# Kernel tuning notes

Hardware: AMD Instinct MI355X
Metric: run time of the kernel (lower is better)

The kernel has to match this reference:

```python
import jax, jax.numpy as jnp
import numpy as np

N, DEG = 20000, 16          # nodes, fixed neighbor-list length
H, C, D, IN = 4, 16, 128, 256  # cluster_heads, num_centroids, hidden_dim, input_dim
NEG_SLOPE = 0.2


def setup_inputs() -> dict:
    key = jax.random.key(0)
    ks = jax.random.split(key, 12)
    s_in = 1.0 / np.sqrt(IN)
    s_h = 1.0 / np.sqrt(D)
    inp = {
        "x_node": jax.random.normal(ks[0], (N, IN), dtype=jnp.float32),
        "adj": jax.random.randint(ks[1], (N, DEG), 0, N, dtype=jnp.int32),
        "epoch": 1,
        # linear layers (torch convention: W [out, in])
        "W1": jax.random.uniform(ks[2], (D, IN), jnp.float32, -s_in, s_in),
        "b1": jax.random.uniform(ks[3], (D,), jnp.float32, -s_in, s_in),
        "W2": jax.random.uniform(ks[4], (D, D), jnp.float32, -s_h, s_h),
        "b2": jax.random.uniform(ks[5], (D,), jnp.float32, -s_h, s_h),
        "W21": jax.random.uniform(ks[6], (D, D), jnp.float32, -s_h, s_h),
        "b21": jax.random.uniform(ks[7], (D,), jnp.float32, -s_h, s_h),
        # centroids: 2*rand-1, shape [H, C*D]
        "centroids": 2.0 * jax.random.uniform(ks[8], (H, C * D), dtype=jnp.float32) - 1.0,
        # headConv: xavier_uniform gain=1.414 on [H, 1]
        "headConv": jax.random.uniform(ks[9], (H, 1), jnp.float32,
                                       -1.414 * np.sqrt(6.0 / (H + 1)),
                                       1.414 * np.sqrt(6.0 / (H + 1))),
    }
    return inp


def _leaky(x):
    return jnp.where(x >= 0, x, NEG_SLOPE * x)


def _cluster_block(h, adj, centroids, headConv):
    # h: [N, D]; adj: [N, deg]; centroids: [H, C*D]; headConv: [H, 1]
    cent = centroids.reshape(H, C, D)
    # squared L2 distance dist[h,c,n] = ||x_n - cent_hc||^2 (norm expansion,
    # avoids the [H,C,N,D] broadcast the torch code materializes)
    hn2 = jnp.sum(h * h, axis=-1)                      # [N]
    cn2 = jnp.sum(cent * cent, axis=-1)                # [H, C]
    cross = jnp.einsum('hcd,nd->hcn', cent, h)         # [H, C, N]
    dist = cn2[..., None] + hn2[None, None, :] - 2.0 * cross
    # nu=1: q = (1 + dist)^-1
    q = 1.0 / (1.0 + dist)                             # [H, C, N]
    # gather neighbor scores per node and normalize over the edge dim
    qn = q[:, :, adj]                                  # [H, C, N, deg]
    qn = qn / jnp.sum(qn, axis=3, keepdims=True)
    # combine heads with headConv, then softmax over edges per centroid
    w = jnp.einsum('hcne,h->nce', qn, headConv[:, 0])  # [N, C, deg]
    w = jax.nn.softmax(w, axis=2)
    # weighted aggregation of neighbor features
    new_feat = jnp.einsum('nce,ned->ncd', w, h[adj])   # [N, C, D]
    return new_feat


def reference(x_node, adj, epoch, W1, b1, W2, b2, W21, b21, centroids, headConv):
    # eval mode: dropout is identity
    x = _leaky(x_node @ W1.T + b1)
    h_prime = _leaky(x @ W2.T + b2)                    # [N, D]
    new_feat = _cluster_block(h_prime, adj, centroids, headConv)
    new_feat = _leaky(new_feat @ W21.T + b21)          # [N, C, D]
    return (h_prime, new_feat)
```

## Files before the change

kernel.cpp:

```cpp
#include <hip/hip_runtime.h>
#include <cstdint>
#include <cstddef>

#define NEG_SLOPE 0.2f

typedef __attribute__((ext_vector_type(8))) short bf16x8;
typedef __attribute__((ext_vector_type(8))) unsigned short u16x8;
typedef __attribute__((ext_vector_type(4))) unsigned short u16x4;
typedef __attribute__((ext_vector_type(4))) float f32x4;
typedef __attribute__((ext_vector_type(2))) float f32x2;

__device__ __forceinline__ float leaky_f(float x) { return x >= 0.f ? x : NEG_SLOPE * x; }

__device__ __forceinline__ unsigned short f2bf(float f) {
    union { float f; uint32_t u; } v; v.f = f;
    return (unsigned short)((v.u + 0x7fffu + ((v.u >> 16) & 1u)) >> 16);
}
__device__ __forceinline__ float bf2f(unsigned short u) {
    union { uint32_t u; float f; } v; v.u = ((uint32_t)u) << 16; return v.f;
}
__device__ __forceinline__ float bfhi(uint32_t w) {
    union { uint32_t u; float f; } v; v.u = w & 0xffff0000u; return v.f;
}
__device__ __forceinline__ float bflo(uint32_t w) {
    union { uint32_t u; float f; } v; v.u = w << 16; return v.f;
}
__device__ __forceinline__ u16x8 cvt8(float4 a, float4 b) {
    u16x8 o;
    o[0] = f2bf(a.x); o[1] = f2bf(a.y); o[2] = f2bf(a.z); o[3] = f2bf(a.w);
    o[4] = f2bf(b.x); o[5] = f2bf(b.y); o[6] = f2bf(b.z); o[7] = f2bf(b.w);
    return o;
}

#if __has_builtin(__builtin_elementwise_fma)
__device__ __forceinline__ f32x2 fma2(f32x2 a, f32x2 b, f32x2 c) {
    return __builtin_elementwise_fma(a, b, c);
}
#else
__device__ __forceinline__ f32x2 fma2(f32x2 a, f32x2 b, f32x2 c) {
    f32x2 r; r[0] = fmaf(a[0], b[0], c[0]); r[1] = fmaf(a[1], b[1], c[1]); return r;
}
#endif

__device__ __forceinline__ float xor32_add(float v) {
    float y = v;
    asm volatile("v_permlane32_swap_b32 %0, %1" : "+v"(y), "+v"(v));
    return v + y;
}

__global__ __launch_bounds__(256)
void pack_kernel(const float* __restrict__ x_node, const float* __restrict__ W1,
                 const float* __restrict__ W2, const float* __restrict__ W21,
                 const float* __restrict__ cent,
                 unsigned short* __restrict__ xb, unsigned short* __restrict__ pw1,
                 unsigned short* __restrict__ pw2, unsigned short* __restrict__ pw3,
                 float* __restrict__ cn2g, int N)
{
    const int bid = blockIdx.x, tid = threadIdx.x;
    if (bid < 36) {
        const int sub = tid >> 6, lane = tid & 63, g = bid * 4 + sub;
        const int l15 = lane & 15, l4 = lane >> 4;
        const float* src; unsigned short* dst;
        if (g < 64) {
            int step = g >> 3, f = g & 7;
            src = W1 + (size_t)(f * 16 + l15) * 256 + step * 32 + l4 * 8;
            dst = pw1 + ((size_t)(step * 8 + f) * 64 + lane) * 8;
        } else if (g < 96) {
            int gg = g - 64, step = gg >> 3, f = gg & 7;
            src = W2 + (size_t)(f * 16 + l15) * 128 + step * 32 + l4 * 8;
            dst = pw2 + ((size_t)(step * 8 + f) * 64 + lane) * 8;
        } else {
            int gg = g - 96, step = gg / 12, f = gg % 12;
            int brow = f * 16 + l15;
            const float* base = (brow < 128) ? (W21 + (size_t)brow * 128)
                                             : (cent + (size_t)(brow - 128) * 128);
            src = base + step * 32 + l4 * 8;
            dst = pw3 + ((size_t)(step * 12 + f) * 64 + lane) * 8;
        }
        float4 a = *reinterpret_cast<const float4*>(src);
        float4 b = *reinterpret_cast<const float4*>(src + 4);
        *reinterpret_cast<u16x8*>(dst) = cvt8(a, b);
    } else if (bid == 36) {
        int r = tid >> 2, c0 = (tid & 3) * 32;
        const float* cr = cent + (size_t)r * 128 + c0;
        float s = 0.f;
#pragma unroll
        for (int q = 0; q < 8; q++) {
            float4 v = *reinterpret_cast<const float4*>(cr + q * 4);
            s += v.x * v.x + v.y * v.y + v.z * v.z + v.w * v.w;
        }
        s += __shfl_xor(s, 1); s += __shfl_xor(s, 2);
        if ((tid & 3) == 0) cn2g[r] = s;
    } else {
        size_t base = (size_t)(bid - 37) * 4096 + (size_t)tid * 16;
        float4 v0 = *reinterpret_cast<const float4*>(x_node + base);
        float4 v1 = *reinterpret_cast<const float4*>(x_node + base + 4);
        float4 v2 = *reinterpret_cast<const float4*>(x_node + base + 8);
        float4 v3 = *reinterpret_cast<const float4*>(x_node + base + 12);
        *reinterpret_cast<u16x8*>(xb + base)     = cvt8(v0, v1);
        *reinterpret_cast<u16x8*>(xb + base + 8) = cvt8(v2, v3);
    }
}

__global__ __launch_bounds__(256)
void fused_gemms(const unsigned short* __restrict__ xb,
                 const unsigned short* __restrict__ pw1, const unsigned short* __restrict__ pw2,
                 const unsigned short* __restrict__ pw3,
                 const float* __restrict__ b1, const float* __restrict__ b2,
                 const float* __restrict__ cn2g,
                 float* __restrict__ h_out, unsigned short* __restrict__ hWb,
                 unsigned short* __restrict__ qtb, int N)
{
    __shared__ __align__(16) short Xs[16 * 136];
    __shared__ __align__(16) float hf32[16 * 132];
    __shared__ __align__(16) unsigned short hWs[16 * 136];
    __shared__ __align__(16) unsigned short qts[16 * 72];
    __shared__ float hn2s[4][16];

    const int tid = threadIdx.x, wave = tid >> 6, lane = tid & 63;
    const int l15 = lane & 15, l4 = lane >> 4;
    const int rowBlk = blockIdx.x * 16;

    f32x4 a0{0.f,0.f,0.f,0.f}, a1{0.f,0.f,0.f,0.f}, a2{0.f,0.f,0.f,0.f};
    {
        const unsigned short* ap = xb + (size_t)(rowBlk + l15) * 256 + l4 * 8;
        const unsigned short* bp = pw1 + (size_t)(wave * 2) * 512 + lane * 8;
#pragma unroll
        for (int k = 0; k < 8; k++) {
            bf16x8 af = *reinterpret_cast<const bf16x8*>(ap + k * 32);
            bf16x8 bf0 = *reinterpret_cast<const bf16x8*>(bp + (size_t)k * 8 * 512);
            bf16x8 bf1 = *reinterpret_cast<const bf16x8*>(bp + (size_t)k * 8 * 512 + 512);
            a0 = __builtin_amdgcn_mfma_f32_16x16x32_bf16(af, bf0, a0, 0, 0, 0);
            a1 = __builtin_amdgcn_mfma_f32_16x16x32_bf16(af, bf1, a1, 0, 0, 0);
        }
        float bia = b1[wave * 32 + l15], bib = b1[wave * 32 + 16 + l15];
#pragma unroll
        for (int j = 0; j < 4; j++) {
            Xs[(l4 * 4 + j) * 136 + wave * 32 + l15]      = (short)f2bf(leaky_f(a0[j] + bia));
            Xs[(l4 * 4 + j) * 136 + wave * 32 + 16 + l15] = (short)f2bf(leaky_f(a1[j] + bib));
        }
    }
    __syncthreads();

    a0 = f32x4{0.f,0.f,0.f,0.f}; a1 = f32x4{0.f,0.f,0.f,0.f};
    const short* xp = &Xs[l15 * 136 + l4 * 8];
    {
        const unsigned short* bp = pw2 + (size_t)(wave * 2) * 512 + lane * 8;
#pragma unroll
        for (int k = 0; k < 4; k++) {
            bf16x8 af = *reinterpret_cast<const bf16x8*>(xp + k * 32);
            bf16x8 bf0 = *reinterpret_cast<const bf16x8*>(bp + (size_t)k * 8 * 512);
            bf16x8 bf1 = *reinterpret_cast<const bf16x8*>(bp + (size_t)k * 8 * 512 + 512);
            a0 = __builtin_amdgcn_mfma_f32_16x16x32_bf16(af, bf0, a0, 0, 0, 0);
            a1 = __builtin_amdgcn_mfma_f32_16x16x32_bf16(af, bf1, a1, 0, 0, 0);
        }
    }
    float hv0[4], hv1[4], pn[4];
    {
        float bia = b2[wave * 32 + l15], bib = b2[wave * 32 + 16 + l15];
#pragma unroll
        for (int j = 0; j < 4; j++) {
            hv0[j] = leaky_f(a0[j] + bia);
            hv1[j] = leaky_f(a1[j] + bib);
            float s = hv0[j] * hv0[j] + hv1[j] * hv1[j];
            s += __shfl_xor(s, 1); s += __shfl_xor(s, 2);
            s += __shfl_xor(s, 4); s += __shfl_xor(s, 8);
            pn[j] = s;
        }
    }
    __syncthreads();

#pragma unroll
    for (int j = 0; j < 4; j++) {
        int r = l4 * 4 + j;
        hf32[r * 132 + wave * 32 + l15]      = hv0[j];
        hf32[r * 132 + wave * 32 + 16 + l15] = hv1[j];
        Xs[r * 136 + wave * 32 + l15]      = (short)f2bf(hv0[j]);
        Xs[r * 136 + wave * 32 + 16 + l15] = (short)f2bf(hv1[j]);
        if (l15 == 0) hn2s[wave][r] = pn[j];
    }
    __syncthreads();

    {
        int r = tid >> 4, c0 = (tid & 15) * 8;
        f32x4 v0 = *reinterpret_cast<const f32x4*>(&hf32[r * 132 + c0]);
        f32x4 v1 = *reinterpret_cast<const f32x4*>(&hf32[r * 132 + c0 + 4]);
        float* dst = h_out + (size_t)(rowBlk + r) * 128 + c0;
        __builtin_nontemporal_store(v0, reinterpret_cast<f32x4*>(dst));
        __builtin_nontemporal_store(v1, reinterpret_cast<f32x4*>(dst + 4));
    }

    a0 = f32x4{0.f,0.f,0.f,0.f}; a1 = f32x4{0.f,0.f,0.f,0.f}; a2 = f32x4{0.f,0.f,0.f,0.f};
    {
        const unsigned short* bp = pw3 + (size_t)(wave * 3) * 512 + lane * 8;
#pragma unroll
        for (int k = 0; k < 4; k++) {
            bf16x8 af = *reinterpret_cast<const bf16x8*>(xp + k * 32);
            bf16x8 bf0 = *reinterpret_cast<const bf16x8*>(bp + (size_t)k * 12 * 512);
            bf16x8 bf1 = *reinterpret_cast<const bf16x8*>(bp + (size_t)k * 12 * 512 + 512);
            bf16x8 bf2 = *reinterpret_cast<const bf16x8*>(bp + (size_t)k * 12 * 512 + 1024);
            a0 = __builtin_amdgcn_mfma_f32_16x16x32_bf16(af, bf0, a0, 0, 0, 0);
            a1 = __builtin_amdgcn_mfma_f32_16x16x32_bf16(af, bf1, a1, 0, 0, 0);
            a2 = __builtin_amdgcn_mfma_f32_16x16x32_bf16(af, bf2, a2, 0, 0, 0);
        }
    }
    {
        float hn2r[4];
#pragma unroll
        for (int j = 0; j < 4; j++)
            hn2r[j] = hn2s[0][l4 * 4 + j] + hn2s[1][l4 * 4 + j]
                    + hn2s[2][l4 * 4 + j] + hn2s[3][l4 * 4 + j];
        f32x4 av[3] = {a0, a1, a2};
#pragma unroll
        for (int ff = 0; ff < 3; ff++) {
            int col = wave * 48 + ff * 16 + l15;
            if (col < 128) {
#pragma unroll
                for (int j = 0; j < 4; j++)
                    hWs[(l4 * 4 + j) * 136 + col] = f2bf(av[ff][j]);
            } else {
                int c2 = col - 128;
                float cn2v = cn2g[c2];
#pragma unroll
                for (int j = 0; j < 4; j++) {
                    float q = 1.f / (1.f + cn2v + hn2r[j] - 2.f * av[ff][j]);
                    qts[(l4 * 4 + j) * 72 + c2] = f2bf(q);
                }
            }
        }
    }
    __syncthreads();

    {
        int r = tid >> 4, c0 = (tid & 15) * 8;
        *reinterpret_cast<u16x8*>(hWb + (size_t)(rowBlk + r) * 128 + c0) =
            *reinterpret_cast<const u16x8*>(&hWs[r * 136 + c0]);
        int cq = (tid & 15) * 4;
        *reinterpret_cast<u16x4*>(qtb + (size_t)(rowBlk + r) * 64 + cq) =
            *reinterpret_cast<const u16x4*>(&qts[r * 72 + cq]);
    }
}

struct PerWaveU {
    union {
        unsigned short qs[1024];
        float wbuf[16][16];
    };
};

__global__ __launch_bounds__(256)
void agg_kernel(const int* __restrict__ adj, const unsigned short* __restrict__ qtb,
                const unsigned short* __restrict__ hWb, const float* __restrict__ b21,
                const float* __restrict__ headConv, float* __restrict__ out1)
{
    __shared__ __align__(16) unsigned short hs[4][16 * 128];
    __shared__ __align__(16) PerWaveU upw[4];

    const int wv = threadIdx.x >> 6, lane = threadIdx.x & 63;
    const int eg = lane >> 4, l15 = lane & 15;
    const int n = blockIdx.x * 4 + wv;

    const int myadj = adj[n * 16 + l15];

#pragma unroll
    for (int i = 0; i < 2; i++) {
        int row = i * 8 + (lane >> 3);
        int nb = __shfl(myadj, row);
        *reinterpret_cast<u16x8*>(&upw[wv].qs[i * 512 + lane * 8]) =
            *reinterpret_cast<const u16x8*>(qtb + (size_t)nb * 64 + (lane & 7) * 8);
    }
#pragma unroll
    for (int i = 0; i < 4; i++) {
        int row = i * 4 + eg;
        int nb = __shfl(myadj, row);
        *reinterpret_cast<u16x8*>(&hs[wv][i * 512 + lane * 8]) =
            *reinterpret_cast<const u16x8*>(hWb + (size_t)nb * 128 + l15 * 8);
    }

    {
        float qv[16];
        float s = 0.f;
#pragma unroll
        for (int e = 0; e < 16; e++) { qv[e] = bf2f(upw[wv].qs[e * 64 + lane]); s += qv[e]; }
        float rs = 1.f / s;
        float conv = headConv[eg];
        float ex[4] = {0.f, 0.f, 0.f, 0.f};
#pragma unroll
        for (int e = 0; e < 16; e++) {
            float v = conv * qv[e] * rs;
            v += __shfl_xor(v, 16);
            v = xor32_add(v);
            float evv = __expf(v);
            bool mine = (eg == (e >> 2));
            ex[e & 3] = mine ? evv : ex[e & 3];
        }
        float ps = ex[0] + ex[1] + ex[2] + ex[3];
        ps += __shfl_xor(ps, 16);
        ps = xor32_add(ps);
        float inv = 1.f / ps;
#pragma unroll
        for (int j = 0; j < 4; j++) upw[wv].wbuf[eg * 4 + j][l15] = ex[j] * inv;
    }

    {
        const int d0 = l15 * 4;
        float bvf[8];
        *reinterpret_cast<float4*>(bvf)     = *reinterpret_cast<const float4*>(b21 + d0);
        *reinterpret_cast<float4*>(bvf + 4) = *reinterpret_cast<const float4*>(b21 + d0 + 64);
        f32x2 acc2[4][4];
#pragma unroll
        for (int jc = 0; jc < 4; jc++) {
            acc2[jc][0] = f32x2{bvf[0], bvf[1]};
            acc2[jc][1] = f32x2{bvf[2], bvf[3]};
            acc2[jc][2] = f32x2{bvf[4], bvf[5]};
            acc2[jc][3] = f32x2{bvf[6], bvf[7]};
        }

#pragma unroll
        for (int e = 0; e < 16; e++) {
            uint2 wlo = *reinterpret_cast<const uint2*>(&hs[wv][e * 128 + d0]);
            uint2 whi = *reinterpret_cast<const uint2*>(&hs[wv][e * 128 + 64 + d0]);
            float w4[4];
            *reinterpret_cast<float4*>(w4) =
                *reinterpret_cast<const float4*>(&upw[wv].wbuf[e][eg * 4]);
            f32x2 hv2[4];
            hv2[0] = f32x2{bflo(wlo.x), bfhi(wlo.x)};
            hv2[1] = f32x2{bflo(wlo.y), bfhi(wlo.y)};
            hv2[2] = f32x2{bflo(whi.x), bfhi(whi.x)};
            hv2[3] = f32x2{bflo(whi.y), bfhi(whi.y)};
#pragma unroll
            for (int jc = 0; jc < 4; jc++) {
                f32x2 w2 = f32x2{w4[jc], w4[jc]};
#pragma unroll
                for (int q = 0; q < 4; q++)
                    acc2[jc][q] = fma2(w2, hv2[q], acc2[jc][q]);
            }
        }

#pragma unroll
        for (int jc = 0; jc < 4; jc++) {
            f32x4 lo, hi;
            lo[0] = leaky_f(acc2[jc][0][0]); lo[1] = leaky_f(acc2[jc][0][1]);
            lo[2] = leaky_f(acc2[jc][1][0]); lo[3] = leaky_f(acc2[jc][1][1]);
            hi[0] = leaky_f(acc2[jc][2][0]); hi[1] = leaky_f(acc2[jc][2][1]);
            hi[2] = leaky_f(acc2[jc][3][0]); hi[3] = leaky_f(acc2[jc][3][1]);
            float* dst = out1 + ((size_t)(n * 16 + eg * 4 + jc)) * 128;
            __builtin_nontemporal_store(lo, reinterpret_cast<f32x4*>(dst + d0));
            __builtin_nontemporal_store(hi, reinterpret_cast<f32x4*>(dst + d0 + 64));
        }
    }
}

extern "C" void kernel_launch(void* const* d_in, const int* in_sizes, int n_in,
                              void* d_out, int out_size, void* d_ws, size_t ws_size,
                              hipStream_t stream)
{
    const float* x_node   = (const float*)d_in[0];
    const int*   adj      = (const int*)  d_in[1];
    const float* W1       = (const float*)d_in[3];
    const float* b1       = (const float*)d_in[4];
    const float* W2       = (const float*)d_in[5];
    const float* b2       = (const float*)d_in[6];
    const float* W21      = (const float*)d_in[7];
    const float* b21      = (const float*)d_in[8];
    const float* cent     = (const float*)d_in[9];
    const float* headConv = (const float*)d_in[10];

    const int N = in_sizes[0] / 256;

    float* h    = (float*)d_out;
    float* out1 = h + (size_t)N * 128;

    unsigned short* xb  = (unsigned short*)d_ws;
    unsigned short* hWb = xb  + (size_t)N * 256;
    unsigned short* qtb = hWb + (size_t)N * 128;
    unsigned short* pw1 = qtb + (size_t)N * 64;
    unsigned short* pw2 = pw1 + 32768;
    unsigned short* pw3 = pw2 + 16384;
    float*          cn2g = (float*)(pw3 + 24576);

    const int xblocks = (N * 256) / 4096;

    pack_kernel<<<37 + xblocks, 256, 0, stream>>>(x_node, W1, W2, W21, cent,
                                                  xb, pw1, pw2, pw3, cn2g, N);
    fused_gemms<<<N / 16, 256, 0, stream>>>(xb, pw1, pw2, pw3, b1, b2, cn2g,
                                            h, hWb, qtb, N);
    agg_kernel<<<N / 4, 256, 0, stream>>>(adj, qtb, hWb, b21, headConv, out1);
}
```

Measured before the change: 64.71 us.

## Process 32 rows per block in fused GEMMs and store outputs directly

Each block of the fused GEMM kernel now covers 32 rows instead of 16, so every weight fragment loaded from global memory feeds two MFMA row tiles. This halves both the weight reloads and the grid size. The shared-memory staging buffers for h, hW and q are also removed, and results are written straight from the MFMA accumulator layout with scalar, non-vectorized global stores. That saves LDS traffic and one barrier, but the 2-4 byte stores are less coalesced, more accumulators raise register pressure, and 625 blocks may underfill the GPU.

```diff
diff --git a/kernel.cpp b/kernel.cpp
--- a/kernel.cpp
+++ b/kernel.cpp
@@ -6,7 +6,6 @@
 
 typedef __attribute__((ext_vector_type(8))) short bf16x8;
 typedef __attribute__((ext_vector_type(8))) unsigned short u16x8;
-typedef __attribute__((ext_vector_type(4))) unsigned short u16x4;
 typedef __attribute__((ext_vector_type(4))) float f32x4;
 typedef __attribute__((ext_vector_type(2))) float f32x2;
 
@@ -111,133 +110,147 @@
                  float* __restrict__ h_out, unsigned short* __restrict__ hWb,
                  unsigned short* __restrict__ qtb, int N)
 {
-    __shared__ __align__(16) short Xs[16 * 136];
-    __shared__ __align__(16) float hf32[16 * 132];
-    __shared__ __align__(16) unsigned short hWs[16 * 136];
-    __shared__ __align__(16) unsigned short qts[16 * 72];
-    __shared__ float hn2s[4][16];
+    __shared__ __align__(16) short Xs[32 * 136];
+    __shared__ float hn2s[4][32];
 
     const int tid = threadIdx.x, wave = tid >> 6, lane = tid & 63;
     const int l15 = lane & 15, l4 = lane >> 4;
-    const int rowBlk = blockIdx.x * 16;
-
-    f32x4 a0{0.f,0.f,0.f,0.f}, a1{0.f,0.f,0.f,0.f}, a2{0.f,0.f,0.f,0.f};
-    {
-        const unsigned short* ap = xb + (size_t)(rowBlk + l15) * 256 + l4 * 8;
+    const int rowBlk = blockIdx.x * 32;
+
+    f32x4 a00{0.f,0.f,0.f,0.f}, a01{0.f,0.f,0.f,0.f}, a10{0.f,0.f,0.f,0.f}, a11{0.f,0.f,0.f,0.f};
+    {
+        const unsigned short* ap0 = xb + (size_t)(rowBlk + l15) * 256 + l4 * 8;
+        const unsigned short* ap1 = ap0 + 16 * 256;
         const unsigned short* bp = pw1 + (size_t)(wave * 2) * 512 + lane * 8;
 #pragma unroll
         for (int k = 0; k < 8; k++) {
-            bf16x8 af = *reinterpret_cast<const bf16x8*>(ap + k * 32);
+            bf16x8 af0 = *reinterpret_cast<const bf16x8*>(ap0 + k * 32);
+            bf16x8 af1 = *reinterpret_cast<const bf16x8*>(ap1 + k * 32);
             bf16x8 bf0 = *reinterpret_cast<const bf16x8*>(bp + (size_t)k * 8 * 512);
             bf16x8 bf1 = *reinterpret_cast<const bf16x8*>(bp + (size_t)k * 8 * 512 + 512);
-            a0 = __builtin_amdgcn_mfma_f32_16x16x32_bf16(af, bf0, a0, 0, 0, 0);
-            a1 = __builtin_amdgcn_mfma_f32_16x16x32_bf16(af, bf1, a1, 0, 0, 0);
+            a00 = __builtin_amdgcn_mfma_f32_16x16x32_bf16(af0, bf0, a00, 0, 0, 0);
+            a01 = __builtin_amdgcn_mfma_f32_16x16x32_bf16(af0, bf1, a01, 0, 0, 0);
+            a10 = __builtin_amdgcn_mfma_f32_16x16x32_bf16(af1, bf0, a10, 0, 0, 0);
+            a11 = __builtin_amdgcn_mfma_f32_16x16x32_bf16(af1, bf1, a11, 0, 0, 0);
         }
         float bia = b1[wave * 32 + l15], bib = b1[wave * 32 + 16 + l15];
 #pragma unroll
         for (int j = 0; j < 4; j++) {
-            Xs[(l4 * 4 + j) * 136 + wave * 32 + l15]      = (short)f2bf(leaky_f(a0[j] + bia));
-            Xs[(l4 * 4 + j) * 136 + wave * 32 + 16 + l15] = (short)f2bf(leaky_f(a1[j] + bib));
+            int r0 = l4 * 4 + j;
+            Xs[r0 * 136 + wave * 32 + l15]             = (short)f2bf(leaky_f(a00[j] + bia));
+            Xs[r0 * 136 + wave * 32 + 16 + l15]        = (short)f2bf(leaky_f(a01[j] + bib));
+            Xs[(r0 + 16) * 136 + wave * 32 + l15]      = (short)f2bf(leaky_f(a10[j] + bia));
+            Xs[(r0 + 16) * 136 + wave * 32 + 16 + l15] = (short)f2bf(leaky_f(a11[j] + bib));
         }
     }
     __syncthreads();
 
-    a0 = f32x4{0.f,0.f,0.f,0.f}; a1 = f32x4{0.f,0.f,0.f,0.f};
-    const short* xp = &Xs[l15 * 136 + l4 * 8];
+    a00 = f32x4{0.f,0.f,0.f,0.f}; a01 = f32x4{0.f,0.f,0.f,0.f};
+    a10 = f32x4{0.f,0.f,0.f,0.f}; a11 = f32x4{0.f,0.f,0.f,0.f};
+    const short* xp0 = &Xs[l15 * 136 + l4 * 8];
+    const short* xp1 = &Xs[(16 + l15) * 136 + l4 * 8];
     {
         const unsigned short* bp = pw2 + (size_t)(wave * 2) * 512 + lane * 8;
 #pragma unroll
         for (int k = 0; k < 4; k++) {
-            bf16x8 af = *reinterpret_cast<const bf16x8*>(xp + k * 32);
+            bf16x8 af0 = *reinterpret_cast<const bf16x8*>(xp0 + k * 32);
+            bf16x8 af1 = *reinterpret_cast<const bf16x8*>(xp1 + k * 32);
             bf16x8 bf0 = *reinterpret_cast<const bf16x8*>(bp + (size_t)k * 8 * 512);
             bf16x8 bf1 = *reinterpret_cast<const bf16x8*>(bp + (size_t)k * 8 * 512 + 512);
-            a0 = __builtin_amdgcn_mfma_f32_16x16x32_bf16(af, bf0, a0, 0, 0, 0);
-            a1 = __builtin_amdgcn_mfma_f32_16x16x32_bf16(af, bf1, a1, 0, 0, 0);
-        }
-    }
-    float hv0[4], hv1[4], pn[4];
+            a00 = __builtin_amdgcn_mfma_f32_16x16x32_bf16(af0, bf0, a00, 0, 0, 0);
+            a01 = __builtin_amdgcn_mfma_f32_16x16x32_bf16(af0, bf1, a01, 0, 0, 0);
+            a10 = __builtin_amdgcn_mfma_f32_16x16x32_bf16(af1, bf0, a10, 0, 0, 0);
+            a11 = __builtin_amdgcn_mfma_f32_16x16x32_bf16(af1, bf1, a11, 0, 0, 0);
+        }
+    }
+    float hv00[4], hv01[4], hv10[4], hv11[4], pn0[4], pn1[4];
     {
         float bia = b2[wave * 32 + l15], bib = b2[wave * 32 + 16 + l15];
 #pragma unroll
         for (int j = 0; j < 4; j++) {
-            hv0[j] = leaky_f(a0[j] + bia);
-            hv1[j] = leaky_f(a1[j] + bib);
-            float s = hv0[j] * hv0[j] + hv1[j] * hv1[j];
-            s += __shfl_xor(s, 1); s += __shfl_xor(s, 2);
-            s += __shfl_xor(s, 4); s += __shfl_xor(s, 8);
-            pn[j] = s;
+            hv00[j] = leaky_f(a00[j] + bia);
+            hv01[j] = leaky_f(a01[j] + bib);
+            hv10[j] = leaky_f(a10[j] + bia);
+            hv11[j] = leaky_f(a11[j] + bib);
+            float s0 = hv00[j] * hv00[j] + hv01[j] * hv01[j];
+            s0 += __shfl_xor(s0, 1); s0 += __shfl_xor(s0, 2);
+            s0 += __shfl_xor(s0, 4); s0 += __shfl_xor(s0, 8);
+            pn0[j] = s0;
+            float s1 = hv10[j] * hv10[j] + hv11[j] * hv11[j];
+            s1 += __shfl_xor(s1, 1); s1 += __shfl_xor(s1, 2);
+            s1 += __shfl_xor(s1, 4); s1 += __shfl_xor(s1, 8);
+            pn1[j] = s1;
         }
     }
     __syncthreads();
 
 #pragma unroll
     for (int j = 0; j < 4; j++) {
-        int r = l4 * 4 + j;
-        hf32[r * 132 + wave * 32 + l15]      = hv0[j];
-        hf32[r * 132 + wave * 32 + 16 + l15] = hv1[j];
-        Xs[r * 136 + wave * 32 + l15]      = (short)f2bf(hv0[j]);
-        Xs[r * 136 + wave * 32 + 16 + l15] = (short)f2bf(hv1[j]);
-        if (l15 == 0) hn2s[wave][r] = pn[j];
+        int r0 = l4 * 4 + j;
+        Xs[r0 * 136 + wave * 32 + l15]             = (short)f2bf(hv00[j]);
+        Xs[r0 * 136 + wave * 32 + 16 + l15]        = (short)f2bf(hv01[j]);
+        Xs[(r0 + 16) * 136 + wave * 32 + l15]      = (short)f2bf(hv10[j]);
+        Xs[(r0 + 16) * 136 + wave * 32 + 16 + l15] = (short)f2bf(hv11[j]);
+        __builtin_nontemporal_store(hv00[j], &h_out[(size_t)(rowBlk + r0) * 128 + wave * 32 + l15]);
+        __builtin_nontemporal_store(hv01[j], &h_out[(size_t)(rowBlk + r0) * 128 + wave * 32 + 16 + l15]);
+        __builtin_nontemporal_store(hv10[j], &h_out[(size_t)(rowBlk + 16 + r0) * 128 + wave * 32 + l15]);
+        __builtin_nontemporal_store(hv11[j], &h_out[(size_t)(rowBlk + 16 + r0) * 128 + wave * 32 + 16 + l15]);
+        if (l15 == 0) { hn2s[wave][r0] = pn0[j]; hn2s[wave][16 + r0] = pn1[j]; }
     }
     __syncthreads();
 
-    {
-        int r = tid >> 4, c0 = (tid & 15) * 8;
-        f32x4 v0 = *reinterpret_cast<const f32x4*>(&hf32[r * 132 + c0]);
-        f32x4 v1 = *reinterpret_cast<const f32x4*>(&hf32[r * 132 + c0 + 4]);
-        float* dst = h_out + (size_t)(rowBlk + r) * 128 + c0;
-        __builtin_nontemporal_store(v0, reinterpret_cast<f32x4*>(dst));
-        __builtin_nontemporal_store(v1, reinterpret_cast<f32x4*>(dst + 4));
-    }
-
-    a0 = f32x4{0.f,0.f,0.f,0.f}; a1 = f32x4{0.f,0.f,0.f,0.f}; a2 = f32x4{0.f,0.f,0.f,0.f};
+    f32x4 c00{0.f,0.f,0.f,0.f}, c01{0.f,0.f,0.f,0.f}, c02{0.f,0.f,0.f,0.f};
+    f32x4 c10{0.f,0.f,0.f,0.f}, c11{0.f,0.f,0.f,0.f}, c12{0.f,0.f,0.f,0.f};
     {
         const unsigned short* bp = pw3 + (size_t)(wave * 3) * 512 + lane * 8;
 #pragma unroll
         for (int k = 0; k < 4; k++) {
-            bf16x8 af = *reinterpret_cast<const bf16x8*>(xp + k * 32);
+            bf16x8 af0 = *reinterpret_cast<const bf16x8*>(xp0 + k * 32);
+            bf16x8 af1 = *reinterpret_cast<const bf16x8*>(xp1 + k * 32);
             bf16x8 bf0 = *reinterpret_cast<const bf16x8*>(bp + (size_t)k * 12 * 512);
             bf16x8 bf1 = *reinterpret_cast<const bf16x8*>(bp + (size_t)k * 12 * 512 + 512);
             bf16x8 bf2 = *reinterpret_cast<const bf16x8*>(bp + (size_t)k * 12 * 512 + 1024);
-            a0 = __builtin_amdgcn_mfma_f32_16x16x32_bf16(af, bf0, a0, 0, 0, 0);
-            a1 = __builtin_amdgcn_mfma_f32_16x16x32_bf16(af, bf1, a1, 0, 0, 0);
-            a2 = __builtin_amdgcn_mfma_f32_16x16x32_bf16(af, bf2, a2, 0, 0, 0);
-        }
-    }
-    {
-        float hn2r[4];
-#pragma unroll
-        for (int j = 0; j < 4; j++)
-            hn2r[j] = hn2s[0][l4 * 4 + j] + hn2s[1][l4 * 4 + j]
-                    + hn2s[2][l4 * 4 + j] + hn2s[3][l4 * 4 + j];
-        f32x4 av[3] = {a0, a1, a2};
+            c00 = __builtin_amdgcn_mfma_f32_16x16x32_bf16(af0, bf0, c00, 0, 0, 0);
+            c01 = __builtin_amdgcn_mfma_f32_16x16x32_bf16(af0, bf1, c01, 0, 0, 0);
+            c02 = __builtin_amdgcn_mfma_f32_16x16x32_bf16(af0, bf2, c02, 0, 0, 0);
+            c10 = __builtin_amdgcn_mfma_f32_16x16x32_bf16(af1, bf0, c10, 0, 0, 0);
+            c11 = __builtin_amdgcn_mfma_f32_16x16x32_bf16(af1, bf1, c11, 0, 0, 0);
+            c12 = __builtin_amdgcn_mfma_f32_16x16x32_bf16(af1, bf2, c12, 0, 0, 0);
+        }
+    }
+    {
+        float hn2r0[4], hn2r1[4];
+#pragma unroll
+        for (int j = 0; j < 4; j++) {
+            int r0 = l4 * 4 + j;
+            hn2r0[j] = hn2s[0][r0] + hn2s[1][r0] + hn2s[2][r0] + hn2s[3][r0];
+            hn2r1[j] = hn2s[0][16 + r0] + hn2s[1][16 + r0] + hn2s[2][16 + r0] + hn2s[3][16 + r0];
+        }
+        f32x4 av0[3] = {c00, c01, c02};
+        f32x4 av1[3] = {c10, c11, c12};
 #pragma unroll
         for (int ff = 0; ff < 3; ff++) {
             int col = wave * 48 + ff * 16 + l15;
             if (col < 128) {
 #pragma unroll
-                for (int j = 0; j < 4; j++)
-                    hWs[(l4 * 4 + j) * 136 + col] = f2bf(av[ff][j]);
+                for (int j = 0; j < 4; j++) {
+                    int gr0 = rowBlk + l4 * 4 + j;
+                    hWb[(size_t)gr0 * 128 + col]        = f2bf(av0[ff][j]);
+                    hWb[(size_t)(gr0 + 16) * 128 + col] = f2bf(av1[ff][j]);
+                }
             } else {
                 int c2 = col - 128;
                 float cn2v = cn2g[c2];
 #pragma unroll
                 for (int j = 0; j < 4; j++) {
-                    float q = 1.f / (1.f + cn2v + hn2r[j] - 2.f * av[ff][j]);
-                    qts[(l4 * 4 + j) * 72 + c2] = f2bf(q);
+                    int gr0 = rowBlk + l4 * 4 + j;
+                    float q0 = 1.f / (1.f + cn2v + hn2r0[j] - 2.f * av0[ff][j]);
+                    float q1 = 1.f / (1.f + cn2v + hn2r1[j] - 2.f * av1[ff][j]);
+                    qtb[(size_t)gr0 * 64 + c2]        = f2bf(q0);
+                    qtb[(size_t)(gr0 + 16) * 64 + c2] = f2bf(q1);
                 }
             }
         }
-    }
-    __syncthreads();
-
-    {
-        int r = tid >> 4, c0 = (tid & 15) * 8;
-        *reinterpret_cast<u16x8*>(hWb + (size_t)(rowBlk + r) * 128 + c0) =
-            *reinterpret_cast<const u16x8*>(&hWs[r * 136 + c0]);
-        int cq = (tid & 15) * 4;
-        *reinterpret_cast<u16x4*>(qtb + (size_t)(rowBlk + r) * 64 + cq) =
-            *reinterpret_cast<const u16x4*>(&qts[r * 72 + cq]);
     }
 }
 
@@ -383,7 +396,7 @@
 
     pack_kernel<<<37 + xblocks, 256, 0, stream>>>(x_node, W1, W2, W21, cent,
                                                   xb, pw1, pw2, pw3, cn2g, N);
-    fused_gemms<<<N / 16, 256, 0, stream>>>(xb, pw1, pw2, pw3, b1, b2, cn2g,
+    fused_gemms<<<N / 32, 256, 0, stream>>>(xb, pw1, pw2, pw3, b1, b2, cn2g,
                                             h, hWb, qtb, N);
     agg_kernel<<<N / 4, 256, 0, stream>>>(adj, qtb, hWb, b21, headConv, out1);
 }
```

Result: no change. 64.06 us (median of 2 runs) (-1.0%).
